# Performance work log

Hardware: AMD Instinct MI355X
Metric: run time of the kernel (lower is better)

The kernel has to match this reference:

```python
import jax, jax.numpy as jnp
import numpy as np

N, E = 40000, 640000
IN_DIM, EDGE_DIM, HID, H1 = 5, 11, 128, 4
NEG_SLOPE = 0.2


def _add_self_loops(ei, ea, n):
    # PyG GATConv default: add_self_loops=True, fill_value='mean' for edge_attr
    loop = jnp.arange(n, dtype=ei.dtype)
    ei2 = jnp.concatenate([ei, jnp.stack([loop, loop])], axis=1)
    ea2 = jnp.concatenate([ea, jnp.broadcast_to(ea.mean(0), (n, ea.shape[1]))], axis=0)
    return ei2, ea2


def _gat(x, ei, ea, W, We, a_src, a_dst, a_edge, b, H, C):
    # Single GATConv layer (eval mode, dropout inactive)
    n = x.shape[0]
    xh = (x @ W).reshape(n, H, C)            # [N,H,C]
    eh = (ea @ We).reshape(-1, H, C)         # [E,H,C]
    src, dst = ei[0], ei[1]
    a_s = (xh * a_src).sum(-1)               # [N,H]
    a_d = (xh * a_dst).sum(-1)               # [N,H]
    alpha = jax.nn.leaky_relu(a_s[src] + a_d[dst] + (eh * a_edge).sum(-1), NEG_SLOPE)  # [E,H]
    amax = jax.ops.segment_max(alpha, dst, num_segments=n)
    ex = jnp.exp(alpha - amax[dst])
    den = jax.ops.segment_sum(ex, dst, num_segments=n)
    w = ex / (den[dst] + 1e-16)              # softmax over inbound edges per dst
    out = jax.ops.segment_sum(xh[src] * w[:, :, None], dst, num_segments=n)  # [N,H,C]
    return out.reshape(n, H * C) + b


def setup_inputs() -> dict:
    key = jax.random.key(0)
    ks = jax.random.split(key, 20)
    s = 0.1
    return {
        "x": jax.random.normal(ks[0], (N, IN_DIM), jnp.float32),
        "edge_index": jax.random.randint(ks[1], (2, E), 0, N),
        "edge_attr": jax.random.normal(ks[2], (E, EDGE_DIM), jnp.float32),
        "W1": jax.random.normal(ks[3], (IN_DIM, H1 * HID), jnp.float32) * s,
        "We1": jax.random.normal(ks[4], (EDGE_DIM, H1 * HID), jnp.float32) * s,
        "a_src1": jax.random.normal(ks[5], (H1, HID), jnp.float32) * s,
        "a_dst1": jax.random.normal(ks[6], (H1, HID), jnp.float32) * s,
        "a_edge1": jax.random.normal(ks[7], (H1, HID), jnp.float32) * s,
        "b1": jnp.zeros((H1 * HID,), jnp.float32),
        # layer 2 (512 -> 128, 1 head)
        "W2": jax.random.normal(ks[8], (H1 * HID, HID), jnp.float32) * s,
        "We2": jax.random.normal(ks[9], (EDGE_DIM, HID), jnp.float32) * s,
        "a_src2": jax.random.normal(ks[10], (1, HID), jnp.float32) * s,
        "a_dst2": jax.random.normal(ks[11], (1, HID), jnp.float32) * s,
        "a_edge2": jax.random.normal(ks[12], (1, HID), jnp.float32) * s,
        "b2": jnp.zeros((HID,), jnp.float32),
        # final linear 128 -> 1
        "Wfc": jax.random.normal(ks[13], (HID, 1), jnp.float32) * s,
        "bfc": jnp.zeros((1,), jnp.float32),
    }


def reference(x, edge_index, edge_attr,
              W1, We1, a_src1, a_dst1, a_edge1, b1,
              W2, We2, a_src2, a_dst2, a_edge2, b2,
              Wfc, bfc):
    ei, ea = _add_self_loops(edge_index, edge_attr, x.shape[0])
    h = jax.nn.relu(_gat(x, ei, ea, W1, We1, a_src1, a_dst1, a_edge1, b1, H1, HID))
    h = jax.nn.relu(_gat(h, ei, ea, W2, We2, a_src2, a_dst2, a_edge2, b2, 1, HID))
    return jax.nn.sigmoid(h @ Wfc + bfc)
```

## Files before the change

### kernel.cpp

```cpp
#include <hip/hip_runtime.h>

#define NN   40000
#define EE   640000
#define IND  5
#define ED   11
#define HIDD 128
#define F1   512
#define PSB  2500

typedef unsigned short u16;
typedef unsigned int   u32;
typedef __attribute__((ext_vector_type(8))) short bf16x8;
typedef __attribute__((ext_vector_type(4))) float f32x4;

__device__ __forceinline__ float bf2f(u16 u) { return __uint_as_float(((u32)u) << 16); }
__device__ __forceinline__ u16 f2bf(float f) {
    u32 u = __float_as_uint(f);
    return (u16)((u + 0x7FFFu + ((u >> 16) & 1u)) >> 16);
}

__device__ __forceinline__ float wsum(float v) {
#pragma unroll
    for (int o = 32; o; o >>= 1) v += __shfl_xor(v, o, 64);
    return v;
}
__device__ __forceinline__ float lrelu(float v) { return v > 0.f ? v : 0.2f * v; }


#define SBLK 256
#define SGRID ((NN + SBLK - 1) / SBLK)
#define PREPG (PSB + 33 + NN / 4)

__global__ void __launch_bounds__(256) k_prep(const int* __restrict__ ei,
                                              int* __restrict__ counts,
                                              int* __restrict__ rank,
                                              float* __restrict__ consts,
                                              const float* __restrict__ We1,
                                              const float* __restrict__ ae1,
                                              const float* __restrict__ We2,
                                              const float* __restrict__ ae2,
                                              const float* __restrict__ W2,
                                              u16* __restrict__ bsw,
                                              const float* __restrict__ x,
                                              const float* __restrict__ W1,
                                              const float* __restrict__ as1,
                                              const float* __restrict__ ad1,
                                              float* __restrict__ aS1,
                                              float* __restrict__ aD1) {
    int bid = blockIdx.x, t = threadIdx.x;
    if (bid < PSB) {
        int i = bid * 256 + t;
        rank[i] = atomicAdd(&counts[ei[EE + i]], 1);
        return;
    }
    if (bid == PSB) {
        if (t < 44) {
            int k = t >> 2, h = t & 3;
            float s = 0.f;
            for (int c = 0; c < HIDD; ++c)
                s += We1[k * F1 + h * HIDD + c] * ae1[h * HIDD + c];
            consts[16 + t] = s;
        }
        if (t >= 48 && t < 48 + ED) {
            int k = t - 48;
            float s = 0.f;
            for (int c = 0; c < HIDD; ++c)
                s += We2[k * HIDD + c] * ae2[c];
            consts[64 + k] = s;
        }
        return;
    }
    if (bid < PSB + 33) {
        int t2 = (bid - (PSB + 1)) * 256 + t;
        if (t2 >= 8192) return;
        int lane = t2 & 63, ks = (t2 >> 6) & 15, nt = t2 >> 10;
        int kbase = ks * 32 + (lane >> 4) * 8;
        int n = nt * 16 + (lane & 15);
        size_t dst = (size_t)t2 * 8;
#pragma unroll
        for (int j = 0; j < 8; ++j)
            bsw[dst + j] = f2bf(W2[(size_t)(kbase + j) * HIDD + n]);
        return;
    }
    int n = (bid - (PSB + 33)) * 4 + (t >> 6);
    int lane = t & 63;
    int c0 = lane * 8, h = lane >> 4;
    const float* xp = x + (size_t)n * IND;
    float x0 = xp[0], x1 = xp[1], x2 = xp[2], x3 = xp[3], x4 = xp[4];
    float p = 0.f, q = 0.f;
#pragma unroll
    for (int j = 0; j < 8; ++j) {
        int c = c0 + j;
        float v = x0 * W1[0 * F1 + c] + x1 * W1[1 * F1 + c] + x2 * W1[2 * F1 + c]
                + x3 * W1[3 * F1 + c] + x4 * W1[4 * F1 + c];
        p += v * as1[c];
        q += v * ad1[c];
    }
#pragma unroll
    for (int o = 1; o <= 8; o <<= 1) {
        p += __shfl_xor(p, o, 64);
        q += __shfl_xor(q, o, 64);
    }
    if ((lane & 15) == 0) {
        aS1[n * 4 + h] = p;
        aD1[n * 4 + h] = q;
    }
}

__global__ void __launch_bounds__(SBLK) k_scan(const int* __restrict__ counts,
                                               int* __restrict__ row_off) {
    __shared__ int sh[SBLK];
    __shared__ int s_boff;
    int t = threadIdx.x, b = blockIdx.x;
    int acc = 0;
    for (int i = t; i < b * SBLK; i += SBLK) acc += counts[i];
    sh[t] = acc;
    __syncthreads();
    for (int o = 128; o; o >>= 1) {
        if (t < o) sh[t] += sh[t + o];
        __syncthreads();
    }
    if (t == 0) s_boff = sh[0];
    __syncthreads();
    int boff = s_boff;
    __syncthreads();
    int i = b * SBLK + t;
    int v = (i < NN) ? counts[i] : 0;
    sh[t] = v;
    __syncthreads();
    for (int o = 1; o < SBLK; o <<= 1) {
        int u = (t >= o) ? sh[t - o] : 0;
        __syncthreads();
        sh[t] += u;
        __syncthreads();
    }
    if (i < NN) row_off[i] = boff + sh[t] - v;
    if (b == 0 && t == 0) row_off[NN] = EE;
}

__global__ void __launch_bounds__(256) k_build(const float* __restrict__ ea,
                                               const int* __restrict__ ei,
                                               const int* __restrict__ rank,
                                               const int* __restrict__ row_off,
                                               const float* __restrict__ consts,
                                               uint4* __restrict__ rec,
                                               float* __restrict__ psum) {
    __shared__ float shf[4 * ED];
    int t = threadIdx.x;
    int i = blockIdx.x * 256 + t;
    int s = ei[i];
    int d = ei[EE + i];
    int pos = row_off[d] + rank[i];
    const float* row = ea + (size_t)i * ED;
    float r[ED];
#pragma unroll
    for (int k = 0; k < ED; ++k) r[k] = row[k];
    float e0 = 0.f, e1 = 0.f, e2 = 0.f, e3 = 0.f, et = 0.f;
#pragma unroll
    for (int k = 0; k < ED; ++k) {
        float a = r[k];
        e0 += a * consts[16 + k * 4 + 0];
        e1 += a * consts[16 + k * 4 + 1];
        e2 += a * consts[16 + k * 4 + 2];
        e3 += a * consts[16 + k * 4 + 3];
        et += a * consts[64 + k];
    }
    uint4 q;
    q.x = (u32)f2bf(e0) | ((u32)f2bf(e1) << 16);
    q.y = (u32)f2bf(e2) | ((u32)f2bf(e3) << 16);
    q.z = (u32)s;
    q.w = __float_as_uint(et);
    rec[pos] = q;
#pragma unroll
    for (int k = 0; k < ED; ++k) r[k] = wsum(r[k]);
    int wv = t >> 6, lane = t & 63;
#pragma unroll
    for (int k = 0; k < ED; ++k)
        if (lane == k) shf[wv * ED + k] = r[k];
    __syncthreads();
    if (t < ED)
        psum[(size_t)blockIdx.x * ED + t] =
            shf[t] + shf[ED + t] + shf[2 * ED + t] + shf[3 * ED + t];
}

__global__ void __launch_bounds__(1024) k_sumred(const float* __restrict__ psum,
                                                 float* __restrict__ consts) {
    __shared__ float sh[16 * ED];
    __shared__ float mean[ED];
    int t = threadIdx.x;
    float acc[ED];
#pragma unroll
    for (int k = 0; k < ED; ++k) acc[k] = 0.f;
    for (int w = t; w < PSB; w += 1024) {
        const float* p = psum + (size_t)w * ED;
#pragma unroll
        for (int k = 0; k < ED; ++k) acc[k] += p[k];
    }
#pragma unroll
    for (int k = 0; k < ED; ++k) acc[k] = wsum(acc[k]);
    int wv = t >> 6, lane = t & 63;
#pragma unroll
    for (int k = 0; k < ED; ++k)
        if (lane == k) sh[wv * ED + k] = acc[k];
    __syncthreads();
    if (t < ED) {
        float m = 0.f;
#pragma unroll
        for (int v = 0; v < 16; ++v) m += sh[v * ED + t];
        mean[t] = m * (1.0f / (float)EE);
    }
    __syncthreads();
    if (t < 4) {
        float s = 0.f;
        for (int k = 0; k < ED; ++k) s += mean[k] * consts[16 + k * 4 + t];
        consts[80 + t] = s;
    }
    if (t == 8) {
        float s = 0.f;
        for (int k = 0; k < ED; ++k) s += mean[k] * consts[64 + k];
        consts[96] = s;
    }
}

__global__ void __launch_bounds__(256) k_agg1(const int* __restrict__ row_off,
                                              const uint4* __restrict__ rec,
                                              const float* __restrict__ aS1,
                                              const float* __restrict__ aD1,
                                              const float* __restrict__ x,
                                              const float* __restrict__ W1,
                                              const float* __restrict__ b1,
                                              const float* __restrict__ consts,
                                              u16* __restrict__ h1) {
    int wv = threadIdx.x >> 6, lane = threadIdx.x & 63;
    int g = lane >> 4, sl = lane & 15;
    int n = blockIdx.x * 16 + wv * 4 + g;
    int s0 = row_off[n], s1 = row_off[n + 1];
    float4 adv = *(const float4*)(aD1 + (size_t)n * 4);
    float z0 = 0.f, z1 = 0.f, z2 = 0.f, z3 = 0.f;
    float xa[4][5];
#pragma unroll
    for (int h = 0; h < 4; ++h)
#pragma unroll
        for (int j = 0; j < 5; ++j) xa[h][j] = 0.f;

    for (int i = s0 + sl; i < s1; i += 16) {
        uint4 q = rec[i];
        int s = (int)q.z;
        float e0 = bf2f((u16)(q.x & 0xFFFF)), e1 = bf2f((u16)(q.x >> 16));
        float e2 = bf2f((u16)(q.y & 0xFFFF)), e3 = bf2f((u16)(q.y >> 16));
        float4 as4 = *(const float4*)(aS1 + (size_t)s * 4);
        const float* xp = x + (size_t)s * IND;
        float x0 = xp[0], x1 = xp[1], x2 = xp[2], x3 = xp[3], x4 = xp[4];
        float ex;
        ex = __expf(lrelu(e0 + as4.x + adv.x)); z0 += ex;
        xa[0][0] += ex * x0; xa[0][1] += ex * x1; xa[0][2] += ex * x2;
        xa[0][3] += ex * x3; xa[0][4] += ex * x4;
        ex = __expf(lrelu(e1 + as4.y + adv.y)); z1 += ex;
        xa[1][0] += ex * x0; xa[1][1] += ex * x1; xa[1][2] += ex * x2;
        xa[1][3] += ex * x3; xa[1][4] += ex * x4;
        ex = __expf(lrelu(e2 + as4.z + adv.z)); z2 += ex;
        xa[2][0] += ex * x0; xa[2][1] += ex * x1; xa[2][2] += ex * x2;
        xa[2][3] += ex * x3; xa[2][4] += ex * x4;
        ex = __expf(lrelu(e3 + as4.w + adv.w)); z3 += ex;
        xa[3][0] += ex * x0; xa[3][1] += ex * x1; xa[3][2] += ex * x2;
        xa[3][3] += ex * x3; xa[3][4] += ex * x4;
    }
    if (sl == 0) {
        float4 as4 = *(const float4*)(aS1 + (size_t)n * 4);
        const float* xp = x + (size_t)n * IND;
        float x0 = xp[0], x1 = xp[1], x2 = xp[2], x3 = xp[3], x4 = xp[4];
        float ex;
        ex = __expf(lrelu(consts[80] + as4.x + adv.x)); z0 += ex;
        xa[0][0] += ex * x0; xa[0][1] += ex * x1; xa[0][2] += ex * x2;
        xa[0][3] += ex * x3; xa[0][4] += ex * x4;
        ex = __expf(lrelu(consts[81] + as4.y + adv.y)); z1 += ex;
        xa[1][0] += ex * x0; xa[1][1] += ex * x1; xa[1][2] += ex * x2;
        xa[1][3] += ex * x3; xa[1][4] += ex * x4;
        ex = __expf(lrelu(consts[82] + as4.z + adv.z)); z2 += ex;
        xa[2][0] += ex * x0; xa[2][1] += ex * x1; xa[2][2] += ex * x2;
        xa[2][3] += ex * x3; xa[2][4] += ex * x4;
        ex = __expf(lrelu(consts[83] + as4.w + adv.w)); z3 += ex;
        xa[3][0] += ex * x0; xa[3][1] += ex * x1; xa[3][2] += ex * x2;
        xa[3][3] += ex * x3; xa[3][4] += ex * x4;
    }
#pragma unroll
    for (int o = 1; o <= 8; o <<= 1) {
        z0 += __shfl_xor(z0, o, 64); z1 += __shfl_xor(z1, o, 64);
        z2 += __shfl_xor(z2, o, 64); z3 += __shfl_xor(z3, o, 64);
#pragma unroll
        for (int h = 0; h < 4; ++h)
#pragma unroll
            for (int j = 0; j < 5; ++j) xa[h][j] += __shfl_xor(xa[h][j], o, 64);
    }
    float zz[4] = {z0, z1, z2, z3};
#pragma unroll
    for (int cb = 0; cb < 4; ++cb) {
        float ih = 1.f / (zz[cb] + 1e-16f);
        int c0 = cb * 128 + sl * 8;
        u32 wp[4];
#pragma unroll
        for (int jj = 0; jj < 4; ++jj) {
            int c = c0 + jj * 2;
            float v0 = (xa[cb][0] * W1[0 * F1 + c] + xa[cb][1] * W1[1 * F1 + c]
                      + xa[cb][2] * W1[2 * F1 + c] + xa[cb][3] * W1[3 * F1 + c]
                      + xa[cb][4] * W1[4 * F1 + c]) * ih;
            float v1 = (xa[cb][0] * W1[0 * F1 + c + 1] + xa[cb][1] * W1[1 * F1 + c + 1]
                      + xa[cb][2] * W1[2 * F1 + c + 1] + xa[cb][3] * W1[3 * F1 + c + 1]
                      + xa[cb][4] * W1[4 * F1 + c + 1]) * ih;
            v0 = fmaxf(v0 + b1[c], 0.f);
            v1 = fmaxf(v1 + b1[c + 1], 0.f);
            wp[jj] = (u32)f2bf(v0) | ((u32)f2bf(v1) << 16);
        }
        uint4 st; st.x = wp[0]; st.y = wp[1]; st.z = wp[2]; st.w = wp[3];
        *(uint4*)(h1 + (size_t)n * F1 + c0) = st;
    }
}

__global__ void __launch_bounds__(256, 2) k_gemm2(const u16* __restrict__ h1,
                                                  const u16* __restrict__ bsw,
                                                  const float* __restrict__ as2,
                                                  const float* __restrict__ ad2,
                                                  u16* __restrict__ xh2,
                                                  float* __restrict__ aS2,
                                                  float* __restrict__ aD2) {
    int tid = threadIdx.x;
    int wv = tid >> 6, lane = tid & 63;
    int tile = blockIdx.x * 4 + wv;
    if (tile >= 2500) return;
    int n0 = tile * 16;
    int mrow = lane & 15, quad = lane >> 4;
    const u16* aptr = h1 + (size_t)(n0 + mrow) * F1 + quad * 8;
    const u16* bbase = bsw + lane * 8;
    f32x4 acc[8];
#pragma unroll
    for (int nt = 0; nt < 8; ++nt) acc[nt] = (f32x4){0.f, 0.f, 0.f, 0.f};

    bf16x8 b0[8], b1v[8];
    bf16x8 af0, af1;
    af0 = *(const bf16x8*)(aptr);
#pragma unroll
    for (int nt = 0; nt < 8; ++nt)
        b0[nt] = *(const bf16x8*)(bbase + nt * 8192);
#pragma unroll
    for (int ks = 0; ks < 16; ++ks) {
        if (ks < 15) {
            af1 = *(const bf16x8*)(aptr + (ks + 1) * 32);
#pragma unroll
            for (int nt = 0; nt < 8; ++nt)
                b1v[nt] = *(const bf16x8*)(bbase + nt * 8192 + (ks + 1) * 512);
        }
#pragma unroll
        for (int nt = 0; nt < 8; ++nt)
            acc[nt] = __builtin_amdgcn_mfma_f32_16x16x32_bf16(af0, b0[nt], acc[nt], 0, 0, 0);
        af0 = af1;
#pragma unroll
        for (int nt = 0; nt < 8; ++nt) b0[nt] = b1v[nt];
    }
    float ps[4] = {0.f, 0.f, 0.f, 0.f}, pd[4] = {0.f, 0.f, 0.f, 0.f};
#pragma unroll
    for (int nt = 0; nt < 8; ++nt) {
        int col = nt * 16 + mrow;
        float sa = as2[col], da = ad2[col];
#pragma unroll
        for (int r = 0; r < 4; ++r) {
            float v = acc[nt][r];
            xh2[(size_t)(n0 + quad * 4 + r) * HIDD + col] = f2bf(v);
            ps[r] += v * sa; pd[r] += v * da;
        }
    }
#pragma unroll
    for (int r = 0; r < 4; ++r) {
#pragma unroll
        for (int o = 1; o <= 8; o <<= 1) {
            ps[r] += __shfl_xor(ps[r], o, 64);
            pd[r] += __shfl_xor(pd[r], o, 64);
        }
        if (mrow == 0) {
            aS2[n0 + quad * 4 + r] = ps[r];
            aD2[n0 + quad * 4 + r] = pd[r];
        }
    }
}

__global__ void __launch_bounds__(256) k_agg2(const int* __restrict__ row_off,
                                              const uint4* __restrict__ rec,
                                              const float* __restrict__ aS2,
                                              const float* __restrict__ aD2,
                                              const u16* __restrict__ xh2,
                                              const float* __restrict__ bias2,
                                              const float* __restrict__ Wfc,
                                              const float* __restrict__ bfc,
                                              const float* __restrict__ consts,
                                              float* __restrict__ out) {
    int n = blockIdx.x * 4 + (threadIdx.x >> 6);
    int t = threadIdx.x & 63;
    int s0 = row_off[n], s1 = row_off[n + 1];
    float adn = aD2[n];
    int g = t >> 4, l = t & 15;
    int c0 = l * 8;
    float z = 0.f;
    float acc[8];
#pragma unroll
    for (int j = 0; j < 8; ++j) acc[j] = 0.f;
    for (int i = s0 + g; i < s1; i += 4) {
        uint4 qe = rec[i];
        int s = (int)qe.z;
        float et2 = __uint_as_float(qe.w);
        float ex = __expf(lrelu(aS2[s] + adn + et2));
        z += ex;
        uint4 q = *(const uint4*)(xh2 + (size_t)s * HIDD + c0);
        acc[0] += ex * bf2f((u16)(q.x & 0xFFFF)); acc[1] += ex * bf2f((u16)(q.x >> 16));
        acc[2] += ex * bf2f((u16)(q.y & 0xFFFF)); acc[3] += ex * bf2f((u16)(q.y >> 16));
        acc[4] += ex * bf2f((u16)(q.z & 0xFFFF)); acc[5] += ex * bf2f((u16)(q.z >> 16));
        acc[6] += ex * bf2f((u16)(q.w & 0xFFFF)); acc[7] += ex * bf2f((u16)(q.w >> 16));
    }
    if (g == 0) {
        float ex = __expf(lrelu(aS2[n] + adn + consts[96]));
        z += ex;
        uint4 q = *(const uint4*)(xh2 + (size_t)n * HIDD + c0);
        acc[0] += ex * bf2f((u16)(q.x & 0xFFFF)); acc[1] += ex * bf2f((u16)(q.x >> 16));
        acc[2] += ex * bf2f((u16)(q.y & 0xFFFF)); acc[3] += ex * bf2f((u16)(q.y >> 16));
        acc[4] += ex * bf2f((u16)(q.z & 0xFFFF)); acc[5] += ex * bf2f((u16)(q.z >> 16));
        acc[6] += ex * bf2f((u16)(q.w & 0xFFFF)); acc[7] += ex * bf2f((u16)(q.w >> 16));
    }
#pragma unroll
    for (int o = 16; o <= 32; o <<= 1) {
        z += __shfl_xor(z, o, 64);
#pragma unroll
        for (int j = 0; j < 8; ++j) acc[j] += __shfl_xor(acc[j], o, 64);
    }
    float inv = 1.f / (z + 1e-16f);
    float p = 0.f;
#pragma unroll
    for (int j = 0; j < 8; ++j) {
        float o = fmaxf(acc[j] * inv + bias2[c0 + j], 0.f);
        p += o * Wfc[c0 + j];
    }
#pragma unroll
    for (int o = 1; o <= 8; o <<= 1) p += __shfl_xor(p, o, 64);
    if (t == 0) {
        float logit = p + bfc[0];
        out[n] = 1.f / (1.f + __expf(-logit));
    }
}

extern "C" void kernel_launch(void* const* d_in, const int* in_sizes, int n_in,
                              void* d_out, int out_size, void* d_ws, size_t ws_size,
                              hipStream_t stream) {
    (void)in_sizes; (void)n_in; (void)out_size; (void)ws_size;
    const float* x   = (const float*)d_in[0];
    const int*   ei  = (const int*)d_in[1];
    const float* ea  = (const float*)d_in[2];
    const float* W1  = (const float*)d_in[3];
    const float* We1 = (const float*)d_in[4];
    const float* as1 = (const float*)d_in[5];
    const float* ad1 = (const float*)d_in[6];
    const float* ae1 = (const float*)d_in[7];
    const float* b1  = (const float*)d_in[8];
    const float* W2  = (const float*)d_in[9];
    const float* We2 = (const float*)d_in[10];
    const float* as2 = (const float*)d_in[11];
    const float* ad2 = (const float*)d_in[12];
    const float* ae2 = (const float*)d_in[13];
    const float* b2v = (const float*)d_in[14];
    const float* Wfc = (const float*)d_in[15];
    const float* bfc = (const float*)d_in[16];
    float* out = (float*)d_out;

    char* ws = (char*)d_ws;
    size_t off = 0;
    auto take = [&](size_t nb) {
        size_t r = off;
        off += (nb + 255) & ~(size_t)255;
        return r;
    };
    float* consts = (float*)(ws + take(1024));
    int*   counts = (int*)(ws + take((size_t)NN * 4));
    size_t zbytes = off;
    int* row_off  = (int*)(ws + take((size_t)(NN + 1) * 4));
    int* rank     = (int*)(ws + take((size_t)EE * 4));
    float* psum   = (float*)(ws + take((size_t)PSB * ED * 4));
    uint4* rec    = (uint4*)(ws + take((size_t)EE * 16));
    float* aS1    = (float*)(ws + take((size_t)NN * 16));
    float* aD1    = (float*)(ws + take((size_t)NN * 16));
    float* aS2    = (float*)(ws + take((size_t)NN * 4));
    float* aD2    = (float*)(ws + take((size_t)NN * 4));
    u16* h1       = (u16*)(ws + take((size_t)NN * F1 * 2));
    u16* xh2      = (u16*)(ws + take((size_t)NN * HIDD * 2));
    u16* w2b      = (u16*)(ws + take((size_t)65536 * 2));

    hipMemsetAsync(ws, 0, zbytes, stream);
    k_prep<<<PREPG, 256, 0, stream>>>(ei, counts, rank, consts, We1, ae1, We2, ae2,
                                      W2, w2b, x, W1, as1, ad1, aS1, aD1);
    k_scan<<<SGRID, SBLK, 0, stream>>>(counts, row_off);
    k_build<<<PSB, 256, 0, stream>>>(ea, ei, rank, row_off, consts, rec, psum);
    k_sumred<<<1, 1024, 0, stream>>>(psum, consts);
    k_agg1<<<NN / 16, 256, 0, stream>>>(row_off, rec, aS1, aD1, x, W1, b1, consts, h1);
    k_gemm2<<<625, 256, 0, stream>>>(h1, w2b, as2, ad2, xh2, aS2, aD2);
    k_agg2<<<NN / 4, 256, 0, stream>>>(row_off, rec, aS2, aD2, xh2, b2v, Wfc, bfc,
                                       consts, out);
}
```

Before: 279.2 us.

## Fuse layer-1 aggregation with layer-2 GEMM via LDS tile; fold attention projections

The layer-1 aggregation now writes each block's 16x512 bf16 hidden tile into swizzled shared memory and runs the layer-2 MFMA GEMM in the same kernel. Each wave computes two of the eight column tiles, and the attention dot products are reduced across waves through shared memory. This removes the 40 MB h1 round trip through global memory and one kernel launch. Separately, the layer-1 source/destination attention scores are precomputed as a 5x4 folded W1·a matrix, so per-node scores become a tiny dot product computed in the scan kernel's extra blocks. The cost is more LDS per block (16 KB), which may lower occupancy during aggregation, and less parallelism per tile in the GEMM.

```diff
diff --git a/kernel.cpp b/kernel.cpp
--- a/kernel.cpp
+++ b/kernel.cpp
@@ -29,7 +29,7 @@
 
 #define SBLK 256
 #define SGRID ((NN + SBLK - 1) / SBLK)
-#define PREPG (PSB + 33 + NN / 4)
+#define PREPG (PSB + 33)
 
 __global__ void __launch_bounds__(256) k_prep(const int* __restrict__ ei,
                                               int* __restrict__ counts,
@@ -41,12 +41,9 @@
                                               const float* __restrict__ ae2,
                                               const float* __restrict__ W2,
                                               u16* __restrict__ bsw,
-                                              const float* __restrict__ x,
                                               const float* __restrict__ W1,
                                               const float* __restrict__ as1,
-                                              const float* __restrict__ ad1,
-                                              float* __restrict__ aS1,
-                                              float* __restrict__ aD1) {
+                                              const float* __restrict__ ad1) {
     int bid = blockIdx.x, t = threadIdx.x;
     if (bid < PSB) {
         int i = bid * 256 + t;
@@ -68,74 +65,87 @@
                 s += We2[k * HIDD + c] * ae2[c];
             consts[64 + k] = s;
         }
+        if (t >= 64 && t < 84) {
+            int idx = t - 64, j = idx >> 2, h = idx & 3;
+            float s = 0.f;
+            for (int c = 0; c < HIDD; ++c)
+                s += W1[j * F1 + h * HIDD + c] * as1[h * HIDD + c];
+            consts[100 + idx] = s;
+        }
+        if (t >= 84 && t < 104) {
+            int idx = t - 84, j = idx >> 2, h = idx & 3;
+            float s = 0.f;
+            for (int c = 0; c < HIDD; ++c)
+                s += W1[j * F1 + h * HIDD + c] * ad1[h * HIDD + c];
+            consts[120 + idx] = s;
+        }
         return;
     }
-    if (bid < PSB + 33) {
-        int t2 = (bid - (PSB + 1)) * 256 + t;
-        if (t2 >= 8192) return;
-        int lane = t2 & 63, ks = (t2 >> 6) & 15, nt = t2 >> 10;
-        int kbase = ks * 32 + (lane >> 4) * 8;
-        int n = nt * 16 + (lane & 15);
-        size_t dst = (size_t)t2 * 8;
-#pragma unroll
-        for (int j = 0; j < 8; ++j)
-            bsw[dst + j] = f2bf(W2[(size_t)(kbase + j) * HIDD + n]);
+    int t2 = (bid - (PSB + 1)) * 256 + t;
+    if (t2 >= 8192) return;
+    int lane = t2 & 63, ks = (t2 >> 6) & 15, nt = t2 >> 10;
+    int kbase = ks * 32 + (lane >> 4) * 8;
+    int n = nt * 16 + (lane & 15);
+    size_t dst = (size_t)t2 * 8;
+#pragma unroll
+    for (int j = 0; j < 8; ++j)
+        bsw[dst + j] = f2bf(W2[(size_t)(kbase + j) * HIDD + n]);
+}
+
+__global__ void __launch_bounds__(SBLK) k_scan(const int* __restrict__ counts,
+                                               int* __restrict__ row_off,
+                                               const float* __restrict__ x,
+                                               const float* __restrict__ consts,
+                                               float* __restrict__ aS1,
+                                               float* __restrict__ aD1) {
+    int t = threadIdx.x, b = blockIdx.x;
+    if (b < SGRID) {
+        __shared__ int sh[SBLK];
+        __shared__ int s_boff;
+        int acc = 0;
+        for (int i = t; i < b * SBLK; i += SBLK) acc += counts[i];
+        sh[t] = acc;
+        __syncthreads();
+        for (int o = 128; o; o >>= 1) {
+            if (t < o) sh[t] += sh[t + o];
+            __syncthreads();
+        }
+        if (t == 0) s_boff = sh[0];
+        __syncthreads();
+        int boff = s_boff;
+        __syncthreads();
+        int i = b * SBLK + t;
+        int v = (i < NN) ? counts[i] : 0;
+        sh[t] = v;
+        __syncthreads();
+        for (int o = 1; o < SBLK; o <<= 1) {
+            int u = (t >= o) ? sh[t - o] : 0;
+            __syncthreads();
+            sh[t] += u;
+            __syncthreads();
+        }
+        if (i < NN) row_off[i] = boff + sh[t] - v;
+        if (b == 0 && t == 0) row_off[NN] = EE;
         return;
     }
-    int n = (bid - (PSB + 33)) * 4 + (t >> 6);
-    int lane = t & 63;
-    int c0 = lane * 8, h = lane >> 4;
+    int n = (b - SGRID) * SBLK + t;
+    if (n >= NN) return;
     const float* xp = x + (size_t)n * IND;
-    float x0 = xp[0], x1 = xp[1], x2 = xp[2], x3 = xp[3], x4 = xp[4];
-    float p = 0.f, q = 0.f;
-#pragma unroll
-    for (int j = 0; j < 8; ++j) {
-        int c = c0 + j;
-        float v = x0 * W1[0 * F1 + c] + x1 * W1[1 * F1 + c] + x2 * W1[2 * F1 + c]
-                + x3 * W1[3 * F1 + c] + x4 * W1[4 * F1 + c];
-        p += v * as1[c];
-        q += v * ad1[c];
-    }
-#pragma unroll
-    for (int o = 1; o <= 8; o <<= 1) {
-        p += __shfl_xor(p, o, 64);
-        q += __shfl_xor(q, o, 64);
-    }
-    if ((lane & 15) == 0) {
-        aS1[n * 4 + h] = p;
-        aD1[n * 4 + h] = q;
-    }
-}
-
-__global__ void __launch_bounds__(SBLK) k_scan(const int* __restrict__ counts,
-                                               int* __restrict__ row_off) {
-    __shared__ int sh[SBLK];
-    __shared__ int s_boff;
-    int t = threadIdx.x, b = blockIdx.x;
-    int acc = 0;
-    for (int i = t; i < b * SBLK; i += SBLK) acc += counts[i];
-    sh[t] = acc;
-    __syncthreads();
-    for (int o = 128; o; o >>= 1) {
-        if (t < o) sh[t] += sh[t + o];
-        __syncthreads();
-    }
-    if (t == 0) s_boff = sh[0];
-    __syncthreads();
-    int boff = s_boff;
-    __syncthreads();
-    int i = b * SBLK + t;
-    int v = (i < NN) ? counts[i] : 0;
-    sh[t] = v;
-    __syncthreads();
-    for (int o = 1; o < SBLK; o <<= 1) {
-        int u = (t >= o) ? sh[t - o] : 0;
-        __syncthreads();
-        sh[t] += u;
-        __syncthreads();
-    }
-    if (i < NN) row_off[i] = boff + sh[t] - v;
-    if (b == 0 && t == 0) row_off[NN] = EE;
+    float xv0 = xp[0], xv1 = xp[1], xv2 = xp[2], xv3 = xp[3], xv4 = xp[4];
+    float4 s4, d4;
+    float* sp = (float*)&s4;
+    float* dp = (float*)&d4;
+#pragma unroll
+    for (int h = 0; h < 4; ++h) {
+        sp[h] = xv0 * consts[100 + 0 * 4 + h] + xv1 * consts[100 + 1 * 4 + h]
+              + xv2 * consts[100 + 2 * 4 + h] + xv3 * consts[100 + 3 * 4 + h]
+              + xv4 * consts[100 + 4 * 4 + h];
+        dp[h] = xv0 * consts[120 + 0 * 4 + h] + xv1 * consts[120 + 1 * 4 + h]
+              + xv2 * consts[120 + 2 * 4 + h] + xv3 * consts[120 + 3 * 4 + h]
+              + xv4 * consts[120 + 4 * 4 + h];
+    }
+    *(float4*)(aS1 + (size_t)n * 4) = s4;
+    *(float4*)(aD1 + (size_t)n * 4) = d4;
 }
 
 __global__ void __launch_bounds__(256) k_build(const float* __restrict__ ea,
@@ -222,18 +232,27 @@
     }
 }
 
-__global__ void __launch_bounds__(256) k_agg1(const int* __restrict__ row_off,
-                                              const uint4* __restrict__ rec,
-                                              const float* __restrict__ aS1,
-                                              const float* __restrict__ aD1,
-                                              const float* __restrict__ x,
-                                              const float* __restrict__ W1,
-                                              const float* __restrict__ b1,
-                                              const float* __restrict__ consts,
-                                              u16* __restrict__ h1) {
+__global__ void __launch_bounds__(256) k_agg1g(const int* __restrict__ row_off,
+                                               const uint4* __restrict__ rec,
+                                               const float* __restrict__ aS1,
+                                               const float* __restrict__ aD1,
+                                               const float* __restrict__ x,
+                                               const float* __restrict__ W1,
+                                               const float* __restrict__ b1,
+                                               const float* __restrict__ consts,
+                                               const u16* __restrict__ bsw,
+                                               const float* __restrict__ as2,
+                                               const float* __restrict__ ad2,
+                                               u16* __restrict__ xh2,
+                                               float* __restrict__ aS2,
+                                               float* __restrict__ aD2) {
+    __shared__ u16 hA[16 * 512];
+    __shared__ float sh_ps[4][16], sh_pd[4][16];
     int wv = threadIdx.x >> 6, lane = threadIdx.x & 63;
     int g = lane >> 4, sl = lane & 15;
-    int n = blockIdx.x * 16 + wv * 4 + g;
+    int row = wv * 4 + g;
+    int n0 = blockIdx.x * 16;
+    int n = n0 + row;
     int s0 = row_off[n], s1 = row_off[n + 1];
     float4 adv = *(const float4*)(aD1 + (size_t)n * 4);
     float z0 = 0.f, z1 = 0.f, z2 = 0.f, z3 = 0.f;
@@ -312,58 +331,51 @@
             wp[jj] = (u32)f2bf(v0) | ((u32)f2bf(v1) << 16);
         }
         uint4 st; st.x = wp[0]; st.y = wp[1]; st.z = wp[2]; st.w = wp[3];
-        *(uint4*)(h1 + (size_t)n * F1 + c0) = st;
-    }
-}
-
-__global__ void __launch_bounds__(256, 2) k_gemm2(const u16* __restrict__ h1,
-                                                  const u16* __restrict__ bsw,
-                                                  const float* __restrict__ as2,
-                                                  const float* __restrict__ ad2,
-                                                  u16* __restrict__ xh2,
-                                                  float* __restrict__ aS2,
-                                                  float* __restrict__ aD2) {
-    int tid = threadIdx.x;
-    int wv = tid >> 6, lane = tid & 63;
-    int tile = blockIdx.x * 4 + wv;
-    if (tile >= 2500) return;
-    int n0 = tile * 16;
+        int cbyte = (cb * 256 + sl * 16) ^ ((row & 7) << 4);
+        *(uint4*)((char*)hA + row * 1024 + cbyte) = st;
+    }
+    __syncthreads();
+
     int mrow = lane & 15, quad = lane >> 4;
-    const u16* aptr = h1 + (size_t)(n0 + mrow) * F1 + quad * 8;
     const u16* bbase = bsw + lane * 8;
-    f32x4 acc[8];
-#pragma unroll
-    for (int nt = 0; nt < 8; ++nt) acc[nt] = (f32x4){0.f, 0.f, 0.f, 0.f};
-
-    bf16x8 b0[8], b1v[8];
-    bf16x8 af0, af1;
-    af0 = *(const bf16x8*)(aptr);
-#pragma unroll
-    for (int nt = 0; nt < 8; ++nt)
-        b0[nt] = *(const bf16x8*)(bbase + nt * 8192);
+    int nt0 = wv * 2;
+    f32x4 acc0 = (f32x4){0.f, 0.f, 0.f, 0.f};
+    f32x4 acc1 = (f32x4){0.f, 0.f, 0.f, 0.f};
+    const char* arow = (const char*)hA + mrow * 1024;
+    int axor = (mrow & 7) << 4;
+    bf16x8 af0 = *(const bf16x8*)(arow + ((quad * 16 + 0) ^ axor));
+    bf16x8 af1;
+    bf16x8 b00 = *(const bf16x8*)(bbase + (size_t)nt0 * 8192);
+    bf16x8 b01 = *(const bf16x8*)(bbase + (size_t)(nt0 + 1) * 8192);
+    bf16x8 n00, n01;
 #pragma unroll
     for (int ks = 0; ks < 16; ++ks) {
         if (ks < 15) {
-            af1 = *(const bf16x8*)(aptr + (ks + 1) * 32);
-#pragma unroll
-            for (int nt = 0; nt < 8; ++nt)
-                b1v[nt] = *(const bf16x8*)(bbase + nt * 8192 + (ks + 1) * 512);
-        }
-#pragma unroll
-        for (int nt = 0; nt < 8; ++nt)
-            acc[nt] = __builtin_amdgcn_mfma_f32_16x16x32_bf16(af0, b0[nt], acc[nt], 0, 0, 0);
-        af0 = af1;
-#pragma unroll
-        for (int nt = 0; nt < 8; ++nt) b0[nt] = b1v[nt];
+            af1 = *(const bf16x8*)(arow + ((quad * 16 + (ks + 1) * 64) ^ axor));
+            n00 = *(const bf16x8*)(bbase + (size_t)nt0 * 8192 + (ks + 1) * 512);
+            n01 = *(const bf16x8*)(bbase + (size_t)(nt0 + 1) * 8192 + (ks + 1) * 512);
+        }
+        acc0 = __builtin_amdgcn_mfma_f32_16x16x32_bf16(af0, b00, acc0, 0, 0, 0);
+        acc1 = __builtin_amdgcn_mfma_f32_16x16x32_bf16(af0, b01, acc1, 0, 0, 0);
+        af0 = af1; b00 = n00; b01 = n01;
     }
     float ps[4] = {0.f, 0.f, 0.f, 0.f}, pd[4] = {0.f, 0.f, 0.f, 0.f};
-#pragma unroll
-    for (int nt = 0; nt < 8; ++nt) {
-        int col = nt * 16 + mrow;
+    {
+        int col = nt0 * 16 + mrow;
         float sa = as2[col], da = ad2[col];
 #pragma unroll
         for (int r = 0; r < 4; ++r) {
-            float v = acc[nt][r];
+            float v = acc0[r];
+            xh2[(size_t)(n0 + quad * 4 + r) * HIDD + col] = f2bf(v);
+            ps[r] += v * sa; pd[r] += v * da;
+        }
+    }
+    {
+        int col = (nt0 + 1) * 16 + mrow;
+        float sa = as2[col], da = ad2[col];
+#pragma unroll
+        for (int r = 0; r < 4; ++r) {
+            float v = acc1[r];
             xh2[(size_t)(n0 + quad * 4 + r) * HIDD + col] = f2bf(v);
             ps[r] += v * sa; pd[r] += v * da;
         }
@@ -376,9 +388,19 @@
             pd[r] += __shfl_xor(pd[r], o, 64);
         }
         if (mrow == 0) {
-            aS2[n0 + quad * 4 + r] = ps[r];
-            aD2[n0 + quad * 4 + r] = pd[r];
-        }
+            sh_ps[wv][quad * 4 + r] = ps[r];
+            sh_pd[wv][quad * 4 + r] = pd[r];
+        }
+    }
+    __syncthreads();
+    int t = threadIdx.x;
+    if (t < 16) {
+        float s = sh_ps[0][t] + sh_ps[1][t] + sh_ps[2][t] + sh_ps[3][t];
+        aS2[n0 + t] = s;
+    } else if (t < 32) {
+        int r = t - 16;
+        float s = sh_pd[0][r] + sh_pd[1][r] + sh_pd[2][r] + sh_pd[3][r];
+        aD2[n0 + r] = s;
     }
 }
 
@@ -485,18 +507,17 @@
     float* aD1    = (float*)(ws + take((size_t)NN * 16));
     float* aS2    = (float*)(ws + take((size_t)NN * 4));
     float* aD2    = (float*)(ws + take((size_t)NN * 4));
-    u16* h1       = (u16*)(ws + take((size_t)NN * F1 * 2));
     u16* xh2      = (u16*)(ws + take((size_t)NN * HIDD * 2));
     u16* w2b      = (u16*)(ws + take((size_t)65536 * 2));
 
     hipMemsetAsync(ws, 0, zbytes, stream);
     k_prep<<<PREPG, 256, 0, stream>>>(ei, counts, rank, consts, We1, ae1, We2, ae2,
-                                      W2, w2b, x, W1, as1, ad1, aS1, aD1);
-    k_scan<<<SGRID, SBLK, 0, stream>>>(counts, row_off);
+                                      W2, w2b, W1, as1, ad1);
+    k_scan<<<SGRID * 2, SBLK, 0, stream>>>(counts, row_off, x, consts, aS1, aD1);
     k_build<<<PSB, 256, 0, stream>>>(ea, ei, rank, row_off, consts, rec, psum);
     k_sumred<<<1, 1024, 0, stream>>>(psum, consts);
-    k_agg1<<<NN / 16, 256, 0, stream>>>(row_off, rec, aS1, aD1, x, W1, b1, consts, h1);
-    k_gemm2<<<625, 256, 0, stream>>>(h1, w2b, as2, ad2, xh2, aS2, aD2);
+    k_agg1g<<<PSB, 256, 0, stream>>>(row_off, rec, aS1, aD1, x, W1, b1, consts,
+                                     w2b, as2, ad2, xh2, aS2, aD2);
     k_agg2<<<NN / 4, 256, 0, stream>>>(row_off, rec, aS2, aD2, xh2, b2v, Wfc, bfc,
                                        consts, out);
 }
```

Measured after the change: 247.6 us. -11.3%, faster.
